# Optimization experiments

Measured on AMD Instinct MI355X. Metric: run time of the kernel, lower is better.

## Reference

```python
import jax, jax.numpy as jnp
import numpy as np
from itertools import combinations

D = 32
N_TRAIN = 50000
N_EVAL = 100000
LOG_2PI = float(np.log(2.0 * np.pi))


def setup_inputs() -> dict:
    key = jax.random.key(0)
    k1, k2 = jax.random.split(key)
    X_train = jax.random.normal(k1, (N_TRAIN, D), dtype=jnp.float32)
    x = jax.random.normal(k2, (N_EVAL, D), dtype=jnp.float32)
    return {"X_train": X_train, "x": x}


def reference(X_train, x):
    """GaussianPMIModel: train() then inv_exp_pmi_dict(x), with the dict's
    columns (null, singles, pairs in combinations order) stacked into one
    (N, 1 + D + C(D,2)) array. Null and singleton interactions are all-ones;
    each pair computes exp(logN_diag(x) - logN_full(x))."""
    d_feat = x.shape[1]
    # --- train(): empirical mean and covariance ---
    mean = jnp.mean(X_train, axis=0)                      # (D,)
    Xc = X_train - mean
    n = X_train.shape[0]
    cov = (Xc.T @ Xc) / (n - 1.0)                         # (D, D)

    # --- pair interactions (|subset| == 2), batched over all P pairs ---
    pairs = np.asarray(list(combinations(range(d_feat), 2)), dtype=np.int32)  # (P, 2)
    P = pairs.shape[0]
    xp = x[:, pairs]                                       # (N, P, 2) gather
    mp = mean[pairs]                                       # (P, 2)
    covp = cov[pairs[:, :, None], pairs[:, None, :]]       # (P, 2, 2)
    var = jnp.diagonal(covp, axis1=-2, axis2=-1)           # (P, 2)

    diff = xp - mp                                         # (N, P, 2)
    # MultivariateNormalDiag(loc=mean, scale_diag=sqrt(var)).log_prob
    lp_diag = (-0.5 * jnp.sum(diff * diff / var, axis=-1)
               - 0.5 * jnp.sum(jnp.log(var), axis=-1)
               - LOG_2PI)                                  # (N, P)

    # MultivariateNormalFullCovariance(loc=mean, cov=covp).log_prob via Cholesky
    L = jnp.linalg.cholesky(covp)                          # (P, 2, 2)
    b = jnp.moveaxis(diff, 0, -1)                          # (P, 2, N)
    z = jax.scipy.linalg.solve_triangular(L, b, lower=True)  # (P, 2, N)
    maha = jnp.sum(z * z, axis=1).T                        # (N, P)
    logdet = 2.0 * jnp.sum(jnp.log(jnp.diagonal(L, axis1=-2, axis2=-1)), axis=-1)  # (P,)
    lp_full = -0.5 * maha - 0.5 * logdet - LOG_2PI         # (N, P)

    pair_vals = jnp.exp(lp_diag - lp_full)                 # (N, P)
    ones = jnp.ones((x.shape[0], 1 + d_feat), dtype=x.dtype)  # null + singles
    return jnp.concatenate([ones, pair_vals], axis=1)      # (N, 1 + D + P)
```

## Files before the change

kernel.cpp:

```cpp
#include <hip/hip_runtime.h>
#include <math.h>


#define D       32
#define NPAIRS  496
#define NTRAIN  50000
#define NEVAL   100000
#define OUTC    529
#define ROWS_PB 50
#define MOM_CHUNK 128


__global__ void zero_ws_kernel(float* ws) {
    int t = blockIdx.x * blockDim.x + threadIdx.x;
    if (t < 560) ws[t] = 0.0f;
}

static __device__ __forceinline__ void emit_sxx(float* ws, int i, int j, float v) {
    if (i > j) return;
    if (i == j) {
        atomicAdd(&ws[32 + i], v);
    } else {
        int p = i * 31 - (i * (i - 1)) / 2 + (j - i - 1);
        atomicAdd(&ws[64 + p], v);
    }
}

__global__ __launch_bounds__(256) void moments_kernel(const float* __restrict__ X,
                                                      float* __restrict__ ws) {
    __shared__ float xs[64 * D];
    __shared__ float sdata[256];
    int t = threadIdx.x;
    int ti = t >> 4, tj = t & 15;
    float a00 = 0.f, a01 = 0.f, a10 = 0.f, a11 = 0.f;
    float colsum = 0.f;
    int base = blockIdx.x * MOM_CHUNK;
    const float2* xs2 = (const float2*)xs;

    for (int tile = 0; tile < MOM_CHUNK; tile += 64) {
        for (int e = t; e < 64 * D; e += 256) {
            int r = e >> 5;
            int row = base + tile + r;
            float v = (row < NTRAIN) ? X[(size_t)row * D + (e & 31)] : 0.0f;
            xs[e] = v;
            colsum += v;
        }
        __syncthreads();
        #pragma unroll 4
        for (int r = 0; r < 64; ++r) {
            float2 xi = xs2[r * 16 + ti];
            float2 xj = xs2[r * 16 + tj];
            a00 += xi.x * xj.x; a01 += xi.x * xj.y;
            a10 += xi.y * xj.x; a11 += xi.y * xj.y;
        }
        __syncthreads();
    }
    sdata[t] = colsum;
    __syncthreads();
    if (t < 32) {
        float tot = 0.0f;
        #pragma unroll
        for (int w = 0; w < 8; ++w) tot += sdata[t + 32 * w];
        atomicAdd(&ws[t], tot);
    }
    int i0 = 2 * ti, i1 = 2 * ti + 1, j0 = 2 * tj, j1 = 2 * tj + 1;
    emit_sxx(ws, i0, j0, a00);
    emit_sxx(ws, i0, j1, a01);
    emit_sxx(ws, i1, j0, a10);
    emit_sxx(ws, i1, j1, a11);
}

__global__ void prep_kernel(float* ws) {
    int t = threadIdx.x;
    const float inv_n = 1.0f / (float)NTRAIN;
    const float inv_nm1 = 1.0f / (float)(NTRAIN - 1);
    if (t < D) ws[3040 + t] = ws[t] * inv_n;
    if (t < NPAIRS) {
        int i = 0, rem = t;
        while (rem >= 31 - i) { rem -= 31 - i; ++i; }
        int j = i + 1 + rem;
        float mi = ws[i] * inv_n, mj = ws[j] * inv_n;
        float vi = (ws[32 + i] - (float)NTRAIN * mi * mi) * inv_nm1;
        float vj = (ws[32 + j] - (float)NTRAIN * mj * mj) * inv_nm1;
        float c  = (ws[64 + t] - (float)NTRAIN * mi * mj) * inv_nm1;
        float det = vi * vj - c * c;
        float invdet = 1.0f / det;
        const float LOG2E = 1.44269504088896340736f;
        ws[560  + t] = 0.5f * c * c * invdet / vi * LOG2E;
        ws[1056 + t] = 0.5f * c * c * invdet / vj * LOG2E;
        ws[1552 + t] = -c * invdet * LOG2E;
        ws[2048 + t] = 0.5f * logf(det / (vi * vj)) * LOG2E;
        ((int*)ws)[2544 + t] = i | (j << 8);
    }
}

struct Coef { float A, B, C, K; int oi, oj; };

static __device__ __forceinline__ Coef load_coef(const float* __restrict__ ws, int c) {
    Coef k;
    if (c < 33) {
        k.A = 0.f; k.B = 0.f; k.C = 0.f; k.K = 0.f; k.oi = 0; k.oj = 0;
    } else {
        int p = c - 33;
        k.A = ws[560  + p];
        k.B = ws[1056 + p];
        k.C = ws[1552 + p];
        k.K = ws[2048 + p];
        int ij = ((const int*)ws)[2544 + p];
        k.oi = ij & 255; k.oj = ij >> 8;
    }
    return k;
}

static __device__ __forceinline__ float pair_val(const Coef& k,
                                                 const float* __restrict__ dxr) {
    float di = dxr[k.oi];
    float dj = dxr[k.oj];
    float e = fmaf(k.A, di * di, fmaf(k.B, dj * dj, fmaf(k.C, di * dj, k.K)));
    return exp2f(e);
}

__global__ __launch_bounds__(256) void pmi_kernel(const float* __restrict__ x,
                                                  const float* __restrict__ ws,
                                                  float* __restrict__ out) {
    __shared__ float smean[D];
    __shared__ float dx[ROWS_PB * D];
    int t = threadIdx.x;
    if (t < D) smean[t] = ws[3040 + t];

    Coef c0 = load_coef(ws, t);
    Coef c1 = load_coef(ws, t + 256);
    bool has3 = (t + 512) < OUTC;
    Coef c2 = load_coef(ws, has3 ? t + 512 : 0);
    __syncthreads();

    int rowbase = blockIdx.x * ROWS_PB;
    const float4* x4 = (const float4*)(x + (size_t)rowbase * D);
    float4* dx4 = (float4*)dx;
    for (int f = t; f < ROWS_PB * D / 4; f += 256) {
        float4 v = x4[f];
        int cb = (f & 7) * 4;
        v.x -= smean[cb];     v.y -= smean[cb + 1];
        v.z -= smean[cb + 2]; v.w -= smean[cb + 3];
        dx4[f] = v;
    }
    __syncthreads();

    float* orow = out + (size_t)rowbase * OUTC;
    const float* dxr = dx;
    #pragma unroll 2
    for (int r = 0; r < ROWS_PB; ++r) {
        orow[t]       = pair_val(c0, dxr);
        orow[t + 256] = pair_val(c1, dxr);
        if (has3) orow[t + 512] = pair_val(c2, dxr);
        orow += OUTC; dxr += D;
    }
}

extern "C" void kernel_launch(void* const* d_in, const int* in_sizes, int n_in,
                              void* d_out, int out_size, void* d_ws, size_t ws_size,
                              hipStream_t stream) {
    const float* X = (const float*)d_in[0];
    const float* x = (const float*)d_in[1];
    float* out = (float*)d_out;
    float* ws  = (float*)d_ws;

    hipLaunchKernelGGL(zero_ws_kernel, dim3(3), dim3(256), 0, stream, ws);
    hipLaunchKernelGGL(moments_kernel, dim3((NTRAIN + MOM_CHUNK - 1) / MOM_CHUNK),
                       dim3(256), 0, stream, X, ws);
    hipLaunchKernelGGL(prep_kernel, dim3(1), dim3(512), 0, stream, ws);
    hipLaunchKernelGGL(pmi_kernel, dim3(NEVAL / ROWS_PB), dim3(256), 0, stream,
                       x, ws, out);
}
```

Before: 286.1 us.

## Replace atomic moment accumulation with per-block partials and a reduction in prep

When the workspace is large enough, the moments pass runs 128 persistent blocks that each write their partial sums and cross-products to a strided partial array instead of issuing atomics. The prep kernel then reduces these partials before computing coefficients. This removes the zeroing kernel and the atomic contention of roughly 391 blocks hitting the same 560 addresses. The cost is a serial reduction of 560x128 floats in a single-block prep kernel and fewer blocks in the moments pass.

```diff
diff --git a/kernel.cpp b/kernel.cpp
--- a/kernel.cpp
+++ b/kernel.cpp
@@ -10,6 +10,67 @@
 #define ROWS_PB 50
 #define MOM_CHUNK 128
 
+#define NB      128
+#define NTILES  ((NTRAIN + 63) / 64)
+
+#define PART_FLOATS 71680
+#define CBASE_BIG   71712
+#define CBASE_SMALL 560
+#define COEF_FLOATS 2512
+
+
+__global__ __launch_bounds__(256) void moments2_kernel(const float* __restrict__ X,
+                                                       float* __restrict__ ws) {
+    __shared__ float xs[64 * D];
+    __shared__ float sdata[256];
+    int t = threadIdx.x;
+    int b = blockIdx.x;
+    int ti = t >> 4, tj = t & 15;
+    float a00 = 0.f, a01 = 0.f, a10 = 0.f, a11 = 0.f;
+    float colsum = 0.f;
+    const float2* xs2 = (const float2*)xs;
+
+    for (int tile = b; tile < NTILES; tile += NB) {
+        int base = tile * 64;
+        for (int e = t; e < 64 * D; e += 256) {
+            int r = e >> 5;
+            int row = base + r;
+            float v = (row < NTRAIN) ? X[(size_t)row * D + (e & 31)] : 0.0f;
+            xs[e] = v;
+            colsum += v;
+        }
+        __syncthreads();
+        #pragma unroll 4
+        for (int r = 0; r < 64; ++r) {
+            float2 xi = xs2[r * 16 + ti];
+            float2 xj = xs2[r * 16 + tj];
+            a00 += xi.x * xj.x; a01 += xi.x * xj.y;
+            a10 += xi.y * xj.x; a11 += xi.y * xj.y;
+        }
+        __syncthreads();
+    }
+    sdata[t] = colsum;
+    __syncthreads();
+    if (t < 32) {
+        float tot = 0.0f;
+        #pragma unroll
+        for (int w = 0; w < 8; ++w) tot += sdata[t + 32 * w];
+        ws[t * NB + b] = tot;
+    }
+    int i0 = 2 * ti, i1 = 2 * ti + 1, j0 = 2 * tj, j1 = 2 * tj + 1;
+    #define EMIT2(i, j, v)                                                   \
+        if ((i) <= (j)) {                                                    \
+            int k = ((i) == (j)) ? (32 + (i))                                \
+                    : (64 + (i) * 31 - ((i) * ((i) - 1)) / 2 + ((j) - (i) - 1)); \
+            ws[k * NB + b] = (v);                                            \
+        }
+    EMIT2(i0, j0, a00)
+    EMIT2(i0, j1, a01)
+    EMIT2(i1, j0, a10)
+    EMIT2(i1, j1, a11)
+    #undef EMIT2
+}
+
 
 __global__ void zero_ws_kernel(float* ws) {
     int t = blockIdx.x * blockDim.x + threadIdx.x;
@@ -70,43 +131,64 @@
     emit_sxx(ws, i1, j1, a11);
 }
 
-__global__ void prep_kernel(float* ws) {
-    int t = threadIdx.x;
+
+__global__ __launch_bounds__(256) void prep2_kernel(float* __restrict__ ws,
+                                                    int from_partials, int cbase) {
+    __shared__ float totals[560];
+    int t = threadIdx.x;
+    if (from_partials) {
+        for (int k = t; k < 560; k += 256) {
+            const float4* p4 = (const float4*)(ws + (size_t)k * NB);
+            float s0 = 0.f, s1 = 0.f, s2 = 0.f, s3 = 0.f;
+            #pragma unroll
+            for (int q = 0; q < NB / 4; ++q) {
+                float4 v = p4[q];
+                s0 += v.x; s1 += v.y; s2 += v.z; s3 += v.w;
+            }
+            totals[k] = (s0 + s1) + (s2 + s3);
+        }
+    } else {
+        for (int k = t; k < 560; k += 256) totals[k] = ws[k];
+    }
+    __syncthreads();
+
     const float inv_n = 1.0f / (float)NTRAIN;
     const float inv_nm1 = 1.0f / (float)(NTRAIN - 1);
-    if (t < D) ws[3040 + t] = ws[t] * inv_n;
-    if (t < NPAIRS) {
-        int i = 0, rem = t;
+    if (t < D) ws[cbase + 2480 + t] = totals[t] * inv_n;
+    for (int p = t; p < NPAIRS; p += 256) {
+        int i = 0, rem = p;
         while (rem >= 31 - i) { rem -= 31 - i; ++i; }
         int j = i + 1 + rem;
-        float mi = ws[i] * inv_n, mj = ws[j] * inv_n;
-        float vi = (ws[32 + i] - (float)NTRAIN * mi * mi) * inv_nm1;
-        float vj = (ws[32 + j] - (float)NTRAIN * mj * mj) * inv_nm1;
-        float c  = (ws[64 + t] - (float)NTRAIN * mi * mj) * inv_nm1;
+        float mi = totals[i] * inv_n, mj = totals[j] * inv_n;
+        float vi = (totals[32 + i] - (float)NTRAIN * mi * mi) * inv_nm1;
+        float vj = (totals[32 + j] - (float)NTRAIN * mj * mj) * inv_nm1;
+        float c  = (totals[64 + p] - (float)NTRAIN * mi * mj) * inv_nm1;
         float det = vi * vj - c * c;
         float invdet = 1.0f / det;
         const float LOG2E = 1.44269504088896340736f;
-        ws[560  + t] = 0.5f * c * c * invdet / vi * LOG2E;
-        ws[1056 + t] = 0.5f * c * c * invdet / vj * LOG2E;
-        ws[1552 + t] = -c * invdet * LOG2E;
-        ws[2048 + t] = 0.5f * logf(det / (vi * vj)) * LOG2E;
-        ((int*)ws)[2544 + t] = i | (j << 8);
-    }
-}
+        ws[cbase + p]        = 0.5f * c * c * invdet / vi * LOG2E;
+        ws[cbase + 496 + p]  = 0.5f * c * c * invdet / vj * LOG2E;
+        ws[cbase + 992 + p]  = -c * invdet * LOG2E;
+        ws[cbase + 1488 + p] = 0.5f * logf(det / (vi * vj)) * LOG2E;
+        ((int*)ws)[cbase + 1984 + p] = i | (j << 8);
+    }
+}
+
 
 struct Coef { float A, B, C, K; int oi, oj; };
 
-static __device__ __forceinline__ Coef load_coef(const float* __restrict__ ws, int c) {
+static __device__ __forceinline__ Coef load_coef(const float* __restrict__ ws,
+                                                 int cbase, int c) {
     Coef k;
     if (c < 33) {
         k.A = 0.f; k.B = 0.f; k.C = 0.f; k.K = 0.f; k.oi = 0; k.oj = 0;
     } else {
         int p = c - 33;
-        k.A = ws[560  + p];
-        k.B = ws[1056 + p];
-        k.C = ws[1552 + p];
-        k.K = ws[2048 + p];
-        int ij = ((const int*)ws)[2544 + p];
+        k.A = ws[cbase + p];
+        k.B = ws[cbase + 496 + p];
+        k.C = ws[cbase + 992 + p];
+        k.K = ws[cbase + 1488 + p];
+        int ij = ((const int*)ws)[cbase + 1984 + p];
         k.oi = ij & 255; k.oj = ij >> 8;
     }
     return k;
@@ -122,16 +204,17 @@
 
 __global__ __launch_bounds__(256) void pmi_kernel(const float* __restrict__ x,
                                                   const float* __restrict__ ws,
-                                                  float* __restrict__ out) {
+                                                  float* __restrict__ out,
+                                                  int cbase) {
     __shared__ float smean[D];
     __shared__ float dx[ROWS_PB * D];
     int t = threadIdx.x;
-    if (t < D) smean[t] = ws[3040 + t];
-
-    Coef c0 = load_coef(ws, t);
-    Coef c1 = load_coef(ws, t + 256);
+    if (t < D) smean[t] = ws[cbase + 2480 + t];
+
+    Coef c0 = load_coef(ws, cbase, t);
+    Coef c1 = load_coef(ws, cbase, t + 256);
     bool has3 = (t + 512) < OUTC;
-    Coef c2 = load_coef(ws, has3 ? t + 512 : 0);
+    Coef c2 = load_coef(ws, cbase, has3 ? t + 512 : 33);
     __syncthreads();
 
     int rowbase = blockIdx.x * ROWS_PB;
@@ -157,6 +240,7 @@
     }
 }
 
+
 extern "C" void kernel_launch(void* const* d_in, const int* in_sizes, int n_in,
                               void* d_out, int out_size, void* d_ws, size_t ws_size,
                               hipStream_t stream) {
@@ -165,10 +249,20 @@
     float* out = (float*)d_out;
     float* ws  = (float*)d_ws;
 
-    hipLaunchKernelGGL(zero_ws_kernel, dim3(3), dim3(256), 0, stream, ws);
-    hipLaunchKernelGGL(moments_kernel, dim3((NTRAIN + MOM_CHUNK - 1) / MOM_CHUNK),
-                       dim3(256), 0, stream, X, ws);
-    hipLaunchKernelGGL(prep_kernel, dim3(1), dim3(512), 0, stream, ws);
-    hipLaunchKernelGGL(pmi_kernel, dim3(NEVAL / ROWS_PB), dim3(256), 0, stream,
-                       x, ws, out);
-}
+    bool big = ws_size >= (size_t)(CBASE_BIG + COEF_FLOATS + 64) * sizeof(float);
+    if (big) {
+        hipLaunchKernelGGL(moments2_kernel, dim3(NB), dim3(256), 0, stream, X, ws);
+        hipLaunchKernelGGL(prep2_kernel, dim3(1), dim3(256), 0, stream,
+                           ws, 1, CBASE_BIG);
+        hipLaunchKernelGGL(pmi_kernel, dim3(NEVAL / ROWS_PB), dim3(256), 0, stream,
+                           x, ws, out, CBASE_BIG);
+    } else {
+        hipLaunchKernelGGL(zero_ws_kernel, dim3(3), dim3(256), 0, stream, ws);
+        hipLaunchKernelGGL(moments_kernel, dim3((NTRAIN + MOM_CHUNK - 1) / MOM_CHUNK),
+                           dim3(256), 0, stream, X, ws);
+        hipLaunchKernelGGL(prep2_kernel, dim3(1), dim3(256), 0, stream,
+                           ws, 0, CBASE_SMALL);
+        hipLaunchKernelGGL(pmi_kernel, dim3(NEVAL / ROWS_PB), dim3(256), 0, stream,
+                           x, ws, out, CBASE_SMALL);
+    }
+}
```

New measurement: 286.2 us. No clear change (+0.0%).
